# Kernel tuning notes

Hardware: AMD Instinct MI355X
Metric: run time of the kernel (lower is better)

Reference implementation:

```python
import jax, jax.numpy as jnp
import numpy as np

D = 1024        # hidden_size = input_size = output_size
E = 8           # num_experts
K = 2           # top-k
TEMP = 1.0      # router temperature


def setup_inputs() -> dict:
    key = jax.random.key(0)
    ks = jax.random.split(key, 7)
    s = 0.02
    x = jax.random.normal(ks[0], (4, 2048, D), dtype=jnp.float32)
    w_router = jax.random.normal(ks[1], (D, E), dtype=jnp.float32) * s
    w1 = jax.random.normal(ks[2], (E, D, D), dtype=jnp.float32) * s
    b1 = jnp.zeros((E, D), dtype=jnp.float32)
    w2 = jax.random.normal(ks[3], (E, D, D), dtype=jnp.float32) * s
    b2 = jnp.zeros((E, D), dtype=jnp.float32)
    return {"x": x, "w_router": w_router, "w1": w1, "b1": b1, "w2": w2, "b2": b2}


def reference(x, w_router, w1, b1, w2, b2):
    B, S, _ = x.shape
    # Router: temperature-scaled logits, softmax, top-k
    logits = jnp.einsum('bsd,de->bse', x, w_router) / TEMP          # [B,S,E]
    probs = jax.nn.softmax(logits, axis=-1)
    top_k_probs, top_k_idx = jax.lax.top_k(probs, K)                # [B,S,K]
    xt = x.reshape(-1, D)                                           # [T,D]
    idx = top_k_idx.reshape(-1, K)                                  # [T,K]
    pk = top_k_probs.reshape(-1, K)                                 # [T,K]
    # Dense expert eval: every expert on every token (faithful to source)
    h = jax.nn.gelu(jnp.einsum('td,edh->eth', xt, w1) + b1[:, None, :])
    expert_out = jnp.einsum('eth,ehd->etd', h, w2) + b2[:, None, :]  # [E,T,D]
    expert_out = jnp.transpose(expert_out, (1, 0, 2))                # [T,E,D]
    # Gather selected experts and combine with routing probs
    sel = jnp.take_along_axis(expert_out, idx[:, :, None], axis=1)   # [T,K,D]
    combined = jnp.sum(sel * pk[:, :, None], axis=1)                 # [T,D]
    return combined.reshape(B, S, D), logits
```

## Files before the change

kernel.cpp:

```cpp
#include <hip/hip_runtime.h>
#include <hip/hip_bf16.h>

#define DH 1024
#define NE 8
#define NT 8192
#define NTK 16384
#define BM 128
#define BN 128
#define BK 64
#define KT (DH / BK)

typedef __bf16 bf16x8 __attribute__((ext_vector_type(8)));
typedef float f32x4 __attribute__((ext_vector_type(4)));
typedef unsigned short u16;
typedef u16 u16x8 __attribute__((ext_vector_type(8)));
typedef u16 u16x4 __attribute__((ext_vector_type(4)));

__device__ __forceinline__ u16 f2bf(float f) {
  union { float f; unsigned u; } v; v.f = f;
  return (u16)((v.u + 0x7fffu + ((v.u >> 16) & 1u)) >> 16);
}
__device__ __forceinline__ float bf2f(u16 h) {
  union { unsigned u; float f; } v; v.u = ((unsigned)h) << 16;
  return v.f;
}
__device__ __forceinline__ float gelu_tanh(float v) {
  float y = 0.7978845608028654f * (v + 0.044715f * v * v * v);
  float t = 1.f - 2.f / (1.f + __expf(2.f * y));
  return 0.5f * v * (1.f + t);
}

__device__ __forceinline__ void gload_lds16(const u16* g, u16* l) {
  __builtin_amdgcn_global_load_lds(
      (const __attribute__((address_space(1))) void*)g,
      (__attribute__((address_space(3))) void*)l, 16, 0, 0);
}

__global__ __launch_bounds__(256) void prep_transpose(
    const float* __restrict__ w1, const float* __restrict__ w2,
    u16* __restrict__ w1t, u16* __restrict__ w2t) {
  __shared__ float tile[64][65];
  int z = blockIdx.z;
  const float* src = (z < NE) ? (w1 + (size_t)z * DH * DH) : (w2 + (size_t)(z - NE) * DH * DH);
  u16* dst = (z < NE) ? (w1t + (size_t)z * DH * DH) : (w2t + (size_t)(z - NE) * DH * DH);
  int d0 = blockIdx.y * 64, n0 = blockIdx.x * 64;
  int tid = threadIdx.x;
  int c = tid & 63, r = tid >> 6;
#pragma unroll
  for (int it = 0; it < 16; ++it) {
    int rr = r + it * 4;
    tile[rr][c] = src[(size_t)(d0 + rr) * DH + n0 + c];
  }
  __syncthreads();
#pragma unroll
  for (int it = 0; it < 16; ++it) {
    int rr = r + it * 4;
    dst[(size_t)(n0 + rr) * DH + d0 + c] = f2bf(tile[c][rr]);
  }
}

__global__ __launch_bounds__(256) void router_kernel(
    const float* __restrict__ x, const float* __restrict__ wr,
    float* __restrict__ logits_out, int* __restrict__ tkidx,
    float* __restrict__ tkp, int* __restrict__ counts,
    u16* __restrict__ xb) {
  __shared__ float wsh[NE][DH + 8];
  __shared__ int hist[NE];
  int tid = threadIdx.x;
  for (int i = tid; i < DH * NE; i += 256) {
    int d = i >> 3, e = i & 7;
    wsh[e][d] = wr[i];
  }
  if (tid < NE) hist[tid] = 0;
  __syncthreads();

  int lane = tid & 63;
  int wv = tid >> 6;
  int t0 = blockIdx.x * 32 + wv * 8;
#pragma unroll 1
  for (int i = 0; i < 8; ++i) {
    int t = t0 + i;
    const float4* xp = (const float4*)(x + (size_t)t * DH);
    u16* xbrow = xb + (size_t)t * DH;
    float a[8] = {0.f, 0.f, 0.f, 0.f, 0.f, 0.f, 0.f, 0.f};
#pragma unroll
    for (int it = 0; it < 4; ++it) {
      float4 xv = xp[it * 64 + lane];
      int d0 = (it * 64 + lane) * 4;
      u16x4 c4;
      c4[0] = f2bf(xv.x); c4[1] = f2bf(xv.y); c4[2] = f2bf(xv.z); c4[3] = f2bf(xv.w);
      *(u16x4*)(xbrow + d0) = c4;
#pragma unroll
      for (int e = 0; e < 8; ++e) {
        float4 w4 = *(const float4*)&wsh[e][d0];
        a[e] += xv.x * w4.x + xv.y * w4.y + xv.z * w4.z + xv.w * w4.w;
      }
    }
#pragma unroll
    for (int off = 32; off; off >>= 1) {
#pragma unroll
      for (int e = 0; e < 8; ++e) a[e] += __shfl_xor(a[e], off, 64);
    }
    if (lane < 8) logits_out[(size_t)t * NE + lane] = a[lane];
    if (lane == 0) {
      float m1 = a[0]; int i1 = 0;
#pragma unroll
      for (int e = 1; e < 8; ++e) if (a[e] > m1) { m1 = a[e]; i1 = e; }
      float m2 = -3.4e38f; int i2 = 0;
#pragma unroll
      for (int e = 0; e < 8; ++e) if (e != i1 && a[e] > m2) { m2 = a[e]; i2 = e; }
      float den = 0.f;
#pragma unroll
      for (int e = 0; e < 8; ++e) den += expf(a[e] - m1);
      tkidx[2 * t] = i1; tkidx[2 * t + 1] = i2;
      tkp[2 * t] = 1.0f / den;
      tkp[2 * t + 1] = expf(m2 - m1) / den;
      atomicAdd(&hist[i1], 1);
      atomicAdd(&hist[i2], 1);
    }
  }
  __syncthreads();
  if (tid < NE) atomicAdd(&counts[tid], hist[tid]);
}

__global__ void offsets_kernel(const int* __restrict__ counts,
                               int* __restrict__ offs, int* __restrict__ cur,
                               int* __restrict__ tmap) {
  if (threadIdx.x == 0) {
    int s = 0;
    for (int e = 0; e < NE; ++e) { offs[e] = s; s += counts[e]; cur[e] = 0; }
    offs[NE] = s;
    int t = 0;
    for (int e = 0; e < NE; ++e)
      for (int m0 = 0; m0 < counts[e]; m0 += BM) {
        tmap[1 + 2 * t] = e; tmap[2 + 2 * t] = m0; ++t;
      }
    tmap[0] = t;
  }
}

__global__ __launch_bounds__(1024) void scatter_kernel(
    const int* __restrict__ tkidx, const float* __restrict__ tkp,
    const int* __restrict__ offs, int* __restrict__ cur,
    int* __restrict__ rows, int* __restrict__ posof, float* __restrict__ pp) {
  __shared__ int h[NE];
  __shared__ int base[NE];
  int tid = threadIdx.x;
  int gid = blockIdx.x * 1024 + tid;
  if (tid < NE) h[tid] = 0;
  __syncthreads();
  int e = tkidx[gid];
  int myrank = atomicAdd(&h[e], 1);
  __syncthreads();
  if (tid < NE) base[tid] = atomicAdd(&cur[tid], h[tid]);
  __syncthreads();
  int pos = offs[e] + base[e] + myrank;
  rows[pos] = gid >> 1;
  posof[gid] = pos;
  pp[pos] = tkp[gid];
}

template <int GELU>
__global__ __launch_bounds__(256, 2) void gemm_kernel(
    const u16* __restrict__ A, const u16* __restrict__ W,
    const float* __restrict__ bias, const int* __restrict__ counts,
    const int* __restrict__ offs, const int* __restrict__ rows,
    const int* __restrict__ tmap, u16* __restrict__ outb) {
  int ty = blockIdx.y;
  if (ty >= tmap[0]) return;
  int e = tmap[1 + 2 * ty];
  int m0 = tmap[2 + 2 * ty];
  int cnt = counts[e];
  int seg = offs[e];
  int n0 = blockIdx.x * BN;

  __shared__ __attribute__((aligned(16))) u16 lds[2][(BM + BN) * BK];

  int tid = threadIdx.x;
  int lane = tid & 63;
  int wv = tid >> 6;

  int srow = tid >> 3;
  int schunk = ((tid & 7) ^ ((tid >> 3) & 7)) * 8;
  const u16* aSrc[4];
  const u16* bSrc[4];
#pragma unroll
  for (int i = 0; i < 4; ++i) {
    int gi = m0 + i * 32 + srow;
    int cl = gi < cnt ? gi : cnt - 1;
    int arow = GELU ? rows[seg + cl] : (seg + cl);
    aSrc[i] = A + (size_t)arow * DH + schunk;
    bSrc[i] = W + (size_t)e * DH * DH + (size_t)(n0 + i * 32 + srow) * DH + schunk;
  }

  auto stage = [&](int d, int k0) {
    u16* base = &lds[d][0];
#pragma unroll
    for (int i = 0; i < 4; ++i) {
      gload_lds16(aSrc[i] + k0, base + (i * 32 + wv * 8) * BK);
      gload_lds16(bSrc[i] + k0, base + BM * BK + (i * 32 + wv * 8) * BK);
    }
  };

  int lr = lane & 15;
  int quad = lane >> 4;
  int sx = lr & 7;
  int k0off = (quad ^ sx) * 8;
  int k1off = ((4 + quad) ^ sx) * 8;
  int wrr = (wv >> 1) * 64, wcc = (wv & 1) * 64;

  f32x4 acc[4][4] = {};

  auto compute = [&](int d) {
    const u16* Ab = &lds[d][0];
    const u16* Bb = &lds[d][BM * BK];
    bf16x8 bfr[2][4];
#pragma unroll
    for (int n = 0; n < 4; ++n) {
      const u16* br = Bb + (size_t)(wcc + n * 16 + lr) * BK;
      bfr[0][n] = *(const bf16x8*)(br + k0off);
      bfr[1][n] = *(const bf16x8*)(br + k1off);
    }
    __builtin_amdgcn_s_setprio(1);
#pragma unroll
    for (int m = 0; m < 4; ++m) {
      const u16* ar = Ab + (size_t)(wrr + m * 16 + lr) * BK;
      bf16x8 a0 = *(const bf16x8*)(ar + k0off);
      bf16x8 a1 = *(const bf16x8*)(ar + k1off);
#pragma unroll
      for (int n = 0; n < 4; ++n) {
        acc[m][n] = __builtin_amdgcn_mfma_f32_16x16x32_bf16(a0, bfr[0][n], acc[m][n], 0, 0, 0);
        acc[m][n] = __builtin_amdgcn_mfma_f32_16x16x32_bf16(a1, bfr[1][n], acc[m][n], 0, 0, 0);
      }
    }
    __builtin_amdgcn_s_setprio(0);
  };

  stage(0, 0);
  stage(1, BK);
#pragma unroll 1
  for (int t = 0; t < KT - 2; ++t) {
    asm volatile("s_waitcnt vmcnt(8)" ::: "memory");
    __builtin_amdgcn_s_barrier();
    asm volatile("" ::: "memory");
    compute(t & 1);
    asm volatile("" ::: "memory");
    __builtin_amdgcn_s_barrier();
    stage(t & 1, (t + 2) * BK);
  }
  asm volatile("s_waitcnt vmcnt(8)" ::: "memory");
  __builtin_amdgcn_s_barrier();
  asm volatile("" ::: "memory");
  compute((KT - 2) & 1);
  asm volatile("s_waitcnt vmcnt(0)" ::: "memory");
  __builtin_amdgcn_s_barrier();
  asm volatile("" ::: "memory");
  compute((KT - 1) & 1);

  int r4 = quad * 4;
  const float* be = bias + (size_t)e * DH;
#pragma unroll
  for (int m = 0; m < 4; ++m) {
#pragma unroll
    for (int n = 0; n < 4; ++n) {
      int col = n0 + wcc + n * 16 + lr;
      float bvv = be[col];
#pragma unroll
      for (int j = 0; j < 4; ++j) {
        int gr = m0 + wrr + m * 16 + r4 + j;
        if (gr < cnt) {
          float v = acc[m][n][j] + bvv;
          if (GELU) v = gelu_tanh(v);
          outb[(size_t)(seg + gr) * DH + col] = f2bf(v);
        }
      }
    }
  }
}

__global__ __launch_bounds__(256) void combine_kernel(
    const u16* __restrict__ eo, const float* __restrict__ tkp,
    const int* __restrict__ posof, float* __restrict__ out) {
  int gid = blockIdx.x * 256 + threadIdx.x;
  int t = gid >> 8;
  int n = (gid & 255) * 4;
  float p0 = tkp[2 * t], p1 = tkp[2 * t + 1];
  int q0 = posof[2 * t], q1 = posof[2 * t + 1];
  u16x4 a = *(const u16x4*)(eo + (size_t)q0 * DH + n);
  u16x4 b = *(const u16x4*)(eo + (size_t)q1 * DH + n);
  float4 o;
  o.x = p0 * bf2f(a[0]) + p1 * bf2f(b[0]);
  o.y = p0 * bf2f(a[1]) + p1 * bf2f(b[1]);
  o.z = p0 * bf2f(a[2]) + p1 * bf2f(b[2]);
  o.w = p0 * bf2f(a[3]) + p1 * bf2f(b[3]);
  *(float4*)(out + (size_t)t * DH + n) = o;
}

extern "C" void kernel_launch(void* const* d_in, const int* in_sizes, int n_in,
                              void* d_out, int out_size, void* d_ws, size_t ws_size,
                              hipStream_t stream) {
  const float* x = (const float*)d_in[0];
  const float* w_router = (const float*)d_in[1];
  const float* w1 = (const float*)d_in[2];
  const float* b1 = (const float*)d_in[3];
  const float* w2 = (const float*)d_in[4];
  const float* b2 = (const float*)d_in[5];
  float* out = (float*)d_out;
  float* logits = out + (size_t)NT * DH;

  char* ws = (char*)d_ws;
  size_t off = 0;
  auto alloc = [&](size_t bytes) -> void* {
    void* p = ws + off;
    off = (off + bytes + 255) & ~(size_t)255;
    return p;
  };
  int* ctrl = (int*)alloc(256);
  int* counts = ctrl;
  int* cur = ctrl + 8;
  int* offs = ctrl + 16;
  int* tmap = (int*)alloc(2048);
  int* tkidx = (int*)alloc((size_t)NTK * 4);
  float* tkp = (float*)alloc((size_t)NTK * 4);
  int* rows = (int*)alloc((size_t)NTK * 4);
  int* posof = (int*)alloc((size_t)NTK * 4);
  float* pp = (float*)alloc((size_t)NTK * 4);
  u16* w1t = (u16*)alloc((size_t)NE * DH * DH * 2);
  u16* w2t = (u16*)alloc((size_t)NE * DH * DH * 2);
  u16* hbuf = (u16*)alloc((size_t)NTK * DH * 2);
  u16* eo = (u16*)alloc((size_t)NTK * DH * 2);
  u16* xb = eo;

  hipMemsetAsync(ctrl, 0, 256, stream);

  prep_transpose<<<dim3(16, 16, 16), 256, 0, stream>>>(w1, w2, w1t, w2t);
  router_kernel<<<NT / 32, 256, 0, stream>>>(x, w_router, logits, tkidx, tkp, counts, xb);
  offsets_kernel<<<1, 64, 0, stream>>>(counts, offs, cur, tmap);
  scatter_kernel<<<NTK / 1024, 1024, 0, stream>>>(tkidx, tkp, offs, cur, rows, posof, pp);
  gemm_kernel<1><<<dim3(8, 136, 1), 256, 0, stream>>>(xb, w1t, b1, counts, offs, rows, tmap, hbuf);
  gemm_kernel<0><<<dim3(8, 136, 1), 256, 0, stream>>>(hbuf, w2t, b2, counts, offs, rows, tmap, eo);
  combine_kernel<<<NT, 256, 0, stream>>>(eo, tkp, posof, out);
}
```

Baseline: 220.5 us.

## Enlarge expert GEMM tiles to 256x256 with 512-thread blocks and vectorize weight transpose

The grouped expert GEMMs move from 128x128 tiles with 4 waves to 256x256 tiles with 8 waves. Each wave now computes a 128x64 sub-tile with 8x4 accumulators, and the A-fragment loads are interleaved in pairs with setprio around each MFMA group. This roughly halves global and LDS operand traffic per FLOP. In exchange it needs 128KB of LDS per block, more accumulator registers, and far fewer blocks (288) than CUs can cleanly balance. Separately, the weight transpose/bf16 conversion now uses float4 loads and 4-wide bf16 stores.

Result: no change. 224.6 us (+1.8%).

```diff
diff --git a/kernel.cpp b/kernel.cpp
--- a/kernel.cpp
+++ b/kernel.cpp
@@ -5,8 +5,8 @@
 #define NE 8
 #define NT 8192
 #define NTK 16384
-#define BM 128
-#define BN 128
+#define BM 256
+#define BN 256
 #define BK 64
 #define KT (DH / BK)
 
@@ -45,17 +45,23 @@
   u16* dst = (z < NE) ? (w1t + (size_t)z * DH * DH) : (w2t + (size_t)(z - NE) * DH * DH);
   int d0 = blockIdx.y * 64, n0 = blockIdx.x * 64;
   int tid = threadIdx.x;
-  int c = tid & 63, r = tid >> 6;
-#pragma unroll
-  for (int it = 0; it < 16; ++it) {
-    int rr = r + it * 4;
-    tile[rr][c] = src[(size_t)(d0 + rr) * DH + n0 + c];
-  }
-  __syncthreads();
-#pragma unroll
-  for (int it = 0; it < 16; ++it) {
-    int rr = r + it * 4;
-    dst[(size_t)(n0 + rr) * DH + d0 + c] = f2bf(tile[c][rr]);
+  int r16 = tid >> 4;
+  int c4 = (tid & 15) * 4;
+#pragma unroll
+  for (int it = 0; it < 4; ++it) {
+    int rr = it * 16 + r16;
+    float4 v = *(const float4*)&src[(size_t)(d0 + rr) * DH + n0 + c4];
+    tile[rr][c4] = v.x; tile[rr][c4 + 1] = v.y;
+    tile[rr][c4 + 2] = v.z; tile[rr][c4 + 3] = v.w;
+  }
+  __syncthreads();
+#pragma unroll
+  for (int it = 0; it < 4; ++it) {
+    int n = it * 16 + r16;
+    u16x4 o;
+    o[0] = f2bf(tile[c4][n]);     o[1] = f2bf(tile[c4 + 1][n]);
+    o[2] = f2bf(tile[c4 + 2][n]); o[3] = f2bf(tile[c4 + 3][n]);
+    *(u16x4*)&dst[(size_t)(n0 + n) * DH + d0 + c4] = o;
   }
 }
 
@@ -161,7 +167,7 @@
 }
 
 template <int GELU>
-__global__ __launch_bounds__(256, 2) void gemm_kernel(
+__global__ __launch_bounds__(512, 2) void gemm_kernel(
     const u16* __restrict__ A, const u16* __restrict__ W,
     const float* __restrict__ bias, const int* __restrict__ counts,
     const int* __restrict__ offs, const int* __restrict__ rows,
@@ -179,26 +185,28 @@
   int tid = threadIdx.x;
   int lane = tid & 63;
   int wv = tid >> 6;
+  int wm = wv >> 2;
+  int wn = wv & 3;
 
   int srow = tid >> 3;
-  int schunk = ((tid & 7) ^ ((tid >> 3) & 7)) * 8;
+  int schunk = ((tid & 7) ^ (srow & 7)) * 8;
   const u16* aSrc[4];
   const u16* bSrc[4];
 #pragma unroll
   for (int i = 0; i < 4; ++i) {
-    int gi = m0 + i * 32 + srow;
+    int gi = m0 + i * 64 + srow;
     int cl = gi < cnt ? gi : cnt - 1;
     int arow = GELU ? rows[seg + cl] : (seg + cl);
     aSrc[i] = A + (size_t)arow * DH + schunk;
-    bSrc[i] = W + (size_t)e * DH * DH + (size_t)(n0 + i * 32 + srow) * DH + schunk;
+    bSrc[i] = W + (size_t)e * DH * DH + (size_t)(n0 + i * 64 + srow) * DH + schunk;
   }
 
   auto stage = [&](int d, int k0) {
     u16* base = &lds[d][0];
 #pragma unroll
     for (int i = 0; i < 4; ++i) {
-      gload_lds16(aSrc[i] + k0, base + (i * 32 + wv * 8) * BK);
-      gload_lds16(bSrc[i] + k0, base + BM * BK + (i * 32 + wv * 8) * BK);
+      gload_lds16(aSrc[i] + k0, base + (i * 64 + wv * 8) * BK);
+      gload_lds16(bSrc[i] + k0, base + BM * BK + (i * 64 + wv * 8) * BK);
     }
   };
 
@@ -207,9 +215,9 @@
   int sx = lr & 7;
   int k0off = (quad ^ sx) * 8;
   int k1off = ((4 + quad) ^ sx) * 8;
-  int wrr = (wv >> 1) * 64, wcc = (wv & 1) * 64;
-
-  f32x4 acc[4][4] = {};
+  int wrr = wm * 128, wcc = wn * 64;
+
+  f32x4 acc[8][4] = {};
 
   auto compute = [&](int d) {
     const u16* Ab = &lds[d][0];
@@ -221,19 +229,24 @@
       bfr[0][n] = *(const bf16x8*)(br + k0off);
       bfr[1][n] = *(const bf16x8*)(br + k1off);
     }
-    __builtin_amdgcn_s_setprio(1);
-#pragma unroll
-    for (int m = 0; m < 4; ++m) {
-      const u16* ar = Ab + (size_t)(wrr + m * 16 + lr) * BK;
-      bf16x8 a0 = *(const bf16x8*)(ar + k0off);
-      bf16x8 a1 = *(const bf16x8*)(ar + k1off);
+#pragma unroll
+    for (int s = 0; s < 4; ++s) {
+      const u16* ar0 = Ab + (size_t)(wrr + (2 * s) * 16 + lr) * BK;
+      const u16* ar1 = Ab + (size_t)(wrr + (2 * s + 1) * 16 + lr) * BK;
+      bf16x8 a00 = *(const bf16x8*)(ar0 + k0off);
+      bf16x8 a01 = *(const bf16x8*)(ar0 + k1off);
+      bf16x8 a10 = *(const bf16x8*)(ar1 + k0off);
+      bf16x8 a11 = *(const bf16x8*)(ar1 + k1off);
+      __builtin_amdgcn_s_setprio(1);
 #pragma unroll
       for (int n = 0; n < 4; ++n) {
-        acc[m][n] = __builtin_amdgcn_mfma_f32_16x16x32_bf16(a0, bfr[0][n], acc[m][n], 0, 0, 0);
-        acc[m][n] = __builtin_amdgcn_mfma_f32_16x16x32_bf16(a1, bfr[1][n], acc[m][n], 0, 0, 0);
+        acc[2 * s][n]     = __builtin_amdgcn_mfma_f32_16x16x32_bf16(a00, bfr[0][n], acc[2 * s][n], 0, 0, 0);
+        acc[2 * s][n]     = __builtin_amdgcn_mfma_f32_16x16x32_bf16(a01, bfr[1][n], acc[2 * s][n], 0, 0, 0);
+        acc[2 * s + 1][n] = __builtin_amdgcn_mfma_f32_16x16x32_bf16(a10, bfr[0][n], acc[2 * s + 1][n], 0, 0, 0);
+        acc[2 * s + 1][n] = __builtin_amdgcn_mfma_f32_16x16x32_bf16(a11, bfr[1][n], acc[2 * s + 1][n], 0, 0, 0);
       }
-    }
-    __builtin_amdgcn_s_setprio(0);
+      __builtin_amdgcn_s_setprio(0);
+    }
   };
 
   stage(0, 0);
@@ -260,7 +273,7 @@
   int r4 = quad * 4;
   const float* be = bias + (size_t)e * DH;
 #pragma unroll
-  for (int m = 0; m < 4; ++m) {
+  for (int m = 0; m < 8; ++m) {
 #pragma unroll
     for (int n = 0; n < 4; ++n) {
       int col = n0 + wcc + n * 16 + lr;
@@ -337,7 +350,7 @@
   router_kernel<<<NT / 32, 256, 0, stream>>>(x, w_router, logits, tkidx, tkp, counts, xb);
   offsets_kernel<<<1, 64, 0, stream>>>(counts, offs, cur, tmap);
   scatter_kernel<<<NTK / 1024, 1024, 0, stream>>>(tkidx, tkp, offs, cur, rows, posof, pp);
-  gemm_kernel<1><<<dim3(8, 136, 1), 256, 0, stream>>>(xb, w1t, b1, counts, offs, rows, tmap, hbuf);
-  gemm_kernel<0><<<dim3(8, 136, 1), 256, 0, stream>>>(hbuf, w2t, b2, counts, offs, rows, tmap, eo);
+  gemm_kernel<1><<<dim3(4, 72, 1), 512, 0, stream>>>(xb, w1t, b1, counts, offs, rows, tmap, hbuf);
+  gemm_kernel<0><<<dim3(4, 72, 1), 512, 0, stream>>>(hbuf, w2t, b2, counts, offs, rows, tmap, eo);
   combine_kernel<<<NT, 256, 0, stream>>>(eo, tkp, posof, out);
 }
```
